# Performance work log

Hardware: AMD Instinct MI355X
Metric: run time of the kernel (lower is better)

## Reference

```python
import math
import jax, jax.numpy as jnp
import numpy as np

L, H, E, D = 12, 12, 768, 64   # stack_size, mh_size, embedding_dim, dim_w_matrices
B, S = 4, 512
EPS = 1e-5


def positional_enc(seq_len, model_dim):
    # faithful: power_ind = 10000 XOR int(2*i/dim)
    i = np.arange(model_dim)
    p = np.bitwise_xor(10000, (2 * i) // model_dim).astype(np.float32)
    pos = np.arange(seq_len, dtype=np.float32)[:, None]
    ang = pos / p[None, :]
    pe = np.where(i % 2 == 0, np.sin(ang), np.cos(ang)).astype(np.float32)
    return jnp.asarray(pe)


def layer_norm(x, g, b):
    mu = jnp.mean(x, axis=-1, keepdims=True)
    var = jnp.mean(jnp.square(x - mu), axis=-1, keepdims=True)
    return (x - mu) * jax.lax.rsqrt(var + EPS) * g + b


def encoder(x, wq, wo, g1, b1, fw, fb, g2, b2):
    # x: [B,S,E]; wq: [H,E,D]; wo: [E,H*D]; fw: [E,E] (torch Linear layout)
    bs = x.shape[0] * x.shape[1]
    nb = x.reshape(bs, E)                              # flatten batch (faithful)
    q = jnp.einsum('ne,hed->hnd', nb, wq)              # q == k == v (bug kept)
    scores = jax.nn.softmax(jnp.einsum('hnd,hmd->hnm', q, q) / math.sqrt(D), axis=-1)
    z = jnp.einsum('hnm,hmd->hnd', scores, q)          # [H,BS,D]
    zc = z.reshape(H * D, bs)                          # per-head view(D,-1) + cat
    mh = (wo @ zc).reshape(x.shape)                    # [B,S,E]
    l1 = layer_norm(x + mh, g1, b1)
    ffn = l1 @ fw.T + fb
    return layer_norm(l1 + ffn, g2, b2)


def setup_inputs() -> dict:
    key = jax.random.key(0)
    ks = jax.random.split(key, 8)

    def xavier(k, shape, fan_in, fan_out):
        lim = math.sqrt(6.0 / (fan_in + fan_out))
        return jax.random.uniform(k, shape, jnp.float32, -lim, lim)

    return {
        'tokens': jax.random.normal(ks[0], (B, S, E), jnp.float32),
        'wq':    xavier(ks[1], (L, H, E, D), E, D),
        'wo':    xavier(ks[2], (L, E, H * D), E, H * D),
        'ln1_g': jnp.ones((L, E), jnp.float32),
        'ln1_b': jnp.zeros((L, E), jnp.float32),
        'ffn_w': xavier(ks[3], (L, E, E), E, E),
        'ffn_b': jnp.zeros((L, E), jnp.float32),
        'ln2_g': jnp.ones((L, E), jnp.float32),
        'ln2_b': jnp.zeros((L, E), jnp.float32),
    }


def reference(tokens, wq, wo, ln1_g, ln1_b, ffn_w, ffn_b, ln2_g, ln2_b):
    pe = positional_enc(tokens.shape[1], tokens.shape[2])
    # faithful: layer 0 applied once on pe+tokens, then ALL layers (0 again) in loop
    x = encoder(pe + tokens, wq[0], wo[0], ln1_g[0], ln1_b[0],
                ffn_w[0], ffn_b[0], ln2_g[0], ln2_b[0])
    for l in range(L):
        x = encoder(x, wq[l], wo[l], ln1_g[l], ln1_b[l],
                    ffn_w[l], ffn_b[l], ln2_g[l], ln2_b[l])
    return x
```

## Files before the change

### kernel.cpp

```cpp
#include <hip/hip_runtime.h>
#include <hip/hip_bf16.h>


#define BS_TOK 2048
#define EMB 768
#define NH 12
#define HD 64
#define WQN (12 * NH * EMB * HD)

typedef __attribute__((ext_vector_type(8))) short bf16x8;
typedef __attribute__((ext_vector_type(4))) float f32x4;

__device__ __forceinline__ short f2bf(float f) {
  union { float f; unsigned u; } v;
  v.f = f;
  unsigned r = (v.u + 0x7FFF + ((v.u >> 16) & 1)) >> 16;
  return (short)(unsigned short)r;
}

#define MFMA16(a, b, c) __builtin_amdgcn_mfma_f32_16x16x32_bf16(a, b, c, 0, 0, 0)
#define SW64(r, k) ((r) * 64 + ((((k) >> 3) ^ ((r) & 7)) << 3) + ((k) & 7))

__global__ __launch_bounds__(256) void cvt_f32_bf16_kernel(const float* __restrict__ src,
                                                           short* __restrict__ dst) {
  int i = (blockIdx.x * 256 + threadIdx.x) * 8;
  float4 a = *(const float4*)(src + i);
  float4 b = *(const float4*)(src + i + 4);
  bf16x8 t;
  t[0] = f2bf(a.x); t[1] = f2bf(a.y); t[2] = f2bf(a.z); t[3] = f2bf(a.w);
  t[4] = f2bf(b.x); t[5] = f2bf(b.y); t[6] = f2bf(b.z); t[7] = f2bf(b.w);
  *(bf16x8*)(dst + i) = t;
}

__global__ __launch_bounds__(256) void wq_trans_kernel(const float* __restrict__ wq,
                                                       short* __restrict__ wqT) {
  __shared__ short T[64 * 64];
  const int et = blockIdx.x;
  const int lh = blockIdx.y;
  const int tid = threadIdx.x;
  const float* src = wq + ((size_t)lh * EMB + et * 64) * HD;
  {
    int r = tid >> 2, c16 = (tid & 3) << 4;
    const float* p = src + r * HD + c16;
    float4 x0 = *(const float4*)(p + 0);
    float4 x1 = *(const float4*)(p + 4);
    float4 x2 = *(const float4*)(p + 8);
    float4 x3 = *(const float4*)(p + 12);
    bf16x8 a, b;
    a[0] = f2bf(x0.x); a[1] = f2bf(x0.y); a[2] = f2bf(x0.z); a[3] = f2bf(x0.w);
    a[4] = f2bf(x1.x); a[5] = f2bf(x1.y); a[6] = f2bf(x1.z); a[7] = f2bf(x1.w);
    b[0] = f2bf(x2.x); b[1] = f2bf(x2.y); b[2] = f2bf(x2.z); b[3] = f2bf(x2.w);
    b[4] = f2bf(x3.x); b[5] = f2bf(x3.y); b[6] = f2bf(x3.z); b[7] = f2bf(x3.w);
    int g = c16 >> 3;
    *(bf16x8*)&T[r * 64 + ((g ^ (r & 7)) << 3)] = a;
    *(bf16x8*)&T[r * 64 + (((g + 1) ^ (r & 7)) << 3)] = b;
  }
  __syncthreads();
  {
    int d = tid >> 2, e16 = (tid & 3) << 4;
    bf16x8 t0, t1;
#pragma unroll
    for (int j = 0; j < 8; ++j) t0[j] = T[SW64(e16 + j, d)];
#pragma unroll
    for (int j = 0; j < 8; ++j) t1[j] = T[SW64(e16 + 8 + j, d)];
    short* q = wqT + ((size_t)lh * HD + d) * EMB + et * 64 + e16;
    *(bf16x8*)(q) = t0;
    *(bf16x8*)(q + 8) = t1;
  }
}

__global__ __launch_bounds__(256) void pe_add_kernel(const float* __restrict__ tok,
                                                     float* __restrict__ X,
                                                     short* __restrict__ Xb) {
  int idx = blockIdx.x * 256 + threadIdx.x;
  int e = idx % EMB;
  int t = idx / EMB;
  int s = t & 511;
  float p = (e < 384) ? 10000.0f : 10001.0f;
  float ang = (float)s / p;
  float pe = (e & 1) ? cosf(ang) : sinf(ang);
  float v = tok[idx] + pe;
  X[idx] = v;
  Xb[idx] = f2bf(v);
}

__device__ __forceinline__ void stage_direct_bf16(const short* __restrict__ src, int ld,
                                                  int row0, int k0, short* dst, int tid) {
  int r = tid >> 2, kb = (tid & 3) << 4;
  const short* p = src + (size_t)(row0 + r) * ld + k0 + kb;
  bf16x8 x0 = *(const bf16x8*)(p);
  bf16x8 x1 = *(const bf16x8*)(p + 8);
  int g = kb >> 3;
  *(bf16x8*)&dst[r * 64 + ((g ^ (r & 7)) << 3)] = x0;
  *(bf16x8*)&dst[r * 64 + (((g + 1) ^ (r & 7)) << 3)] = x1;
}

__device__ __forceinline__ void stage_trans_bf16(const short* __restrict__ src, int ld,
                                                 int k0, int col0, short* dst, int tid) {
  int kk = tid >> 2, nb = (tid & 3) << 4;
  const short* p = src + (size_t)(k0 + kk) * ld + col0 + nb;
  bf16x8 x0 = *(const bf16x8*)(p + 0);
  bf16x8 x1 = *(const bf16x8*)(p + 8);
#pragma unroll
  for (int j = 0; j < 8; ++j) dst[SW64(nb + j, kk)] = x0[j];
#pragma unroll
  for (int j = 0; j < 8; ++j) dst[SW64(nb + 8 + j, kk)] = x1[j];
}

#define GEMM_TILE_COMPUTE(As, Bs, acc)                                              \
  {                                                                                 \
    _Pragma("unroll") for (int s = 0; s < 2; ++s) {                                 \
      int ra = (w << 4) + l15;                                                      \
      bf16x8 af = *(const bf16x8*)&As[ra * 64 + ((((s << 2) + quad) ^ (ra & 7)) << 3)]; \
      _Pragma("unroll") for (int nt = 0; nt < 4; ++nt) {                            \
        int rb = (nt << 4) + l15;                                                   \
        bf16x8 bf = *(const bf16x8*)&Bs[rb * 64 + ((((s << 2) + quad) ^ (rb & 7)) << 3)]; \
        acc[nt] = MFMA16(af, bf, acc[nt]);                                          \
      }                                                                             \
    }                                                                               \
  }

__global__ __launch_bounds__(256) void gemm_q_kernel(const short* __restrict__ Xb,
                                                     const short* __restrict__ WqT,
                                                     short* __restrict__ Qo,
                                                     short* __restrict__ Qt) {
  __shared__ short As[64 * 64];
  __shared__ short Bs[64 * 64];
  const int m0 = blockIdx.x * 64;
  const int h = blockIdx.y;
  const int tid = threadIdx.x;
  const int w = tid >> 6, lane = tid & 63, l15 = lane & 15, quad = lane >> 4;
  const short* wqh = WqT + (size_t)h * (HD * EMB);
  f32x4 acc[4] = {(f32x4){0, 0, 0, 0}, (f32x4){0, 0, 0, 0},
                  (f32x4){0, 0, 0, 0}, (f32x4){0, 0, 0, 0}};
  for (int k0 = 0; k0 < EMB; k0 += 64) {
    stage_direct_bf16(Xb, EMB, m0, k0, As, tid);
    stage_direct_bf16(wqh, EMB, 0, k0, Bs, tid);
    __syncthreads();
    GEMM_TILE_COMPUTE(As, Bs, acc);
    __syncthreads();
  }
  short* qo = Qo + (size_t)h * (BS_TOK * HD);
#pragma unroll
  for (int nt = 0; nt < 4; ++nt)
#pragma unroll
    for (int r = 0; r < 4; ++r) {
      short v = f2bf(acc[nt][r]);
      int tokr = (w << 4) + (quad << 2) + r;
      int d = (nt << 4) + l15;
      qo[(size_t)(m0 + tokr) * HD + d] = v;
      As[SW64(tokr, d)] = v;
    }
  __syncthreads();
  {
    int d = tid >> 2, tok0 = (tid & 3) << 4;
    bf16x8 t0, t1;
#pragma unroll
    for (int j = 0; j < 8; ++j) t0[j] = As[SW64(tok0 + j, d)];
#pragma unroll
    for (int j = 0; j < 8; ++j) t1[j] = As[SW64(tok0 + 8 + j, d)];
    short* qt = Qt + (size_t)h * (HD * BS_TOK) + (size_t)d * BS_TOK + m0 + tok0;
    *(bf16x8*)(qt) = t0;
    *(bf16x8*)(qt + 8) = t1;
  }
}

__global__ __launch_bounds__(128) void attn_mfma_kernel(const short* __restrict__ Q,
                                                        const short* __restrict__ Qt,
                                                        float* __restrict__ Opart,
                                                        float* __restrict__ Lpart) {
  __shared__ short Ks[64 * 64];
  __shared__ short Vt[64 * 64];
  __shared__ short Pw[2 * 16 * 64];
  const int h = blockIdx.y;
  const int q0 = blockIdx.x * 32;
  const int kt0 = blockIdx.z * 16;
  const int tid = threadIdx.x;
  const int lane = tid & 63;
  const int wv = tid >> 6;
  const int l15 = lane & 15;
  const int quad = lane >> 4;
  const short* Qh = Q + (size_t)h * (BS_TOK * HD);
  const short* Qth = Qt + (size_t)h * (HD * BS_TOK);
  short* myP = Pw + wv * 16 * 64;

  bf16x8 qf[2];
  {
    const short* qp = Qh + (size_t)(q0 + wv * 16 + l15) * HD + quad * 8;
    qf[0] = *(const bf16x8*)(qp);
    qf[1] = *(const bf16x8*)(qp + 32);
  }

  f32x4 o[4];
  float lp[4] = {0.f, 0.f, 0.f, 0.f};
#pragma unroll
  for (int r = 0; r < 4; ++r) o[r] = (f32x4){0.f, 0.f, 0.f, 0.f};

  bf16x8 kreg[4], vreg[4];
#pragma unroll
  for (int i = 0; i < 4; ++i) {
    int c = i * 128 + tid;
    kreg[i] = *(const bf16x8*)(Qh + kt0 * 4096 + c * 8);
    vreg[i] = *(const bf16x8*)(Qth + (c >> 3) * BS_TOK + kt0 * 64 + (c & 7) * 8);
  }

  for (int kt = 0; kt < 16; ++kt) {
    __syncthreads();
#pragma unroll
    for (int i = 0; i < 4; ++i) {
      int c = i * 128 + tid, row = c >> 3, g = c & 7;
      *(bf16x8*)&Ks[row * 64 + ((g ^ (row & 7)) << 3)] = kreg[i];
      *(bf16x8*)&Vt[row * 64 + ((g ^ (row & 7)) << 3)] = vreg[i];
    }
    __syncthreads();
    if (kt < 15) {
      int gt = kt0 + kt + 1;
#pragma unroll
      for (int i = 0; i < 4; ++i) {
        int c = i * 128 + tid;
        kreg[i] = *(const bf16x8*)(Qh + gt * 4096 + c * 8);
        vreg[i] = *(const bf16x8*)(Qth + (c >> 3) * BS_TOK + gt * 64 + (c & 7) * 8);
      }
    }

    f32x4 s[4];
#pragma unroll
    for (int ct = 0; ct < 4; ++ct) {
      f32x4 acc = (f32x4){0.f, 0.f, 0.f, 0.f};
#pragma unroll
      for (int ks = 0; ks < 2; ++ks) {
        int row = ct * 16 + l15;
        int c = ks * 4 + quad;
        bf16x8 kf = *(const bf16x8*)(&Ks[row * 64 + ((c ^ (row & 7)) << 3)]);
        acc = MFMA16(qf[ks], kf, acc);
      }
      s[ct] = acc;
    }

#pragma unroll
    for (int ct = 0; ct < 4; ++ct)
#pragma unroll
      for (int r = 0; r < 4; ++r) {
        float p = __expf(s[ct][r] * 0.125f);
        lp[r] += p;
        myP[SW64(quad * 4 + r, ct * 16 + l15)] = f2bf(p);
      }

#pragma unroll
    for (int ks = 0; ks < 2; ++ks) {
      int c = ks * 4 + quad;
      bf16x8 pf = *(const bf16x8*)(&myP[l15 * 64 + ((c ^ (l15 & 7)) << 3)]);
#pragma unroll
      for (int dt = 0; dt < 4; ++dt) {
        int row = dt * 16 + l15;
        bf16x8 vf = *(const bf16x8*)(&Vt[row * 64 + ((c ^ (row & 7)) << 3)]);
        o[dt] = MFMA16(pf, vf, o[dt]);
      }
    }
  }

#pragma unroll
  for (int r = 0; r < 4; ++r) {
    float t = lp[r];
#pragma unroll
    for (int d = 1; d < 16; d <<= 1) t += __shfl_xor(t, d, 64);
    lp[r] = t;
  }
  float* Oh = Opart + ((size_t)blockIdx.z * NH + h) * (size_t)(BS_TOK * HD);
  float* Lh = Lpart + ((size_t)blockIdx.z * NH + h) * BS_TOK;
#pragma unroll
  for (int r = 0; r < 4; ++r) {
    int qrow = q0 + wv * 16 + quad * 4 + r;
#pragma unroll
    for (int dt = 0; dt < 4; ++dt)
      Oh[(size_t)qrow * HD + dt * 16 + l15] = o[dt][r];
    if (l15 == 0) Lh[qrow] = lp[r];
  }
}

__global__ __launch_bounds__(256) void attn_combine_kernel(const float* __restrict__ Op,
                                                           const float* __restrict__ Lp,
                                                           short* __restrict__ Z) {
  const int NBH = NH * BS_TOK * HD;
  int idx = blockIdx.x * 256 + threadIdx.x;
  float o = Op[idx] + Op[idx + NBH];
  int hq = idx >> 6;
  float l = Lp[hq] + Lp[hq + NH * BS_TOK];
  Z[idx] = f2bf(o / l);
}

__global__ __launch_bounds__(256) void gemm_out_kernel(const short* __restrict__ Wob,
                                                       const short* __restrict__ Zc,
                                                       float* __restrict__ MH) {
  __shared__ short As[64 * 64];
  __shared__ short Bs[64 * 64];
  const int n0 = blockIdx.x * 64;
  const int m0 = blockIdx.y * 64;
  const int tid = threadIdx.x;
  const int w = tid >> 6, lane = tid & 63, l15 = lane & 15, quad = lane >> 4;
  f32x4 acc[4] = {(f32x4){0, 0, 0, 0}, (f32x4){0, 0, 0, 0},
                  (f32x4){0, 0, 0, 0}, (f32x4){0, 0, 0, 0}};
  for (int k0 = 0; k0 < EMB; k0 += 64) {
    stage_direct_bf16(Wob, EMB, m0, k0, As, tid);
    stage_trans_bf16(Zc, BS_TOK, k0, n0, Bs, tid);
    __syncthreads();
    GEMM_TILE_COMPUTE(As, Bs, acc);
    __syncthreads();
  }
#pragma unroll
  for (int nt = 0; nt < 4; ++nt)
#pragma unroll
    for (int r = 0; r < 4; ++r)
      MH[(size_t)(m0 + (w << 4) + (quad << 2) + r) * BS_TOK + n0 + (nt << 4) + l15] =
          acc[nt][r];
}

__global__ __launch_bounds__(256) void gemm_ffn_kernel(const short* __restrict__ L1b,
                                                       const short* __restrict__ Fwb,
                                                       const float* __restrict__ Fb,
                                                       float* __restrict__ Out) {
  __shared__ short As[64 * 64];
  __shared__ short Bs[64 * 64];
  const int m0 = blockIdx.x * 64;
  const int n0 = blockIdx.y * 64;
  const int tid = threadIdx.x;
  const int w = tid >> 6, lane = tid & 63, l15 = lane & 15, quad = lane >> 4;
  f32x4 acc[4] = {(f32x4){0, 0, 0, 0}, (f32x4){0, 0, 0, 0},
                  (f32x4){0, 0, 0, 0}, (f32x4){0, 0, 0, 0}};
  for (int k0 = 0; k0 < EMB; k0 += 64) {
    stage_direct_bf16(L1b, EMB, m0, k0, As, tid);
    stage_direct_bf16(Fwb, EMB, n0, k0, Bs, tid);
    __syncthreads();
    GEMM_TILE_COMPUTE(As, Bs, acc);
    __syncthreads();
  }
#pragma unroll
  for (int nt = 0; nt < 4; ++nt) {
    float bias = Fb[n0 + (nt << 4) + l15];
#pragma unroll
    for (int r = 0; r < 4; ++r)
      Out[(size_t)(m0 + (w << 4) + (quad << 2) + r) * EMB + n0 + (nt << 4) + l15] =
          acc[nt][r] + bias;
  }
}

__global__ __launch_bounds__(256) void ln_kernel(const float* __restrict__ Xa,
                                                 const float* __restrict__ Xb,
                                                 const float* __restrict__ g,
                                                 const float* __restrict__ bb,
                                                 float* __restrict__ Out,
                                                 short* __restrict__ Outb) {
  __shared__ float red[4];
  const int t = blockIdx.x;
  const int tid = threadIdx.x;
  float v[3];
  float s = 0.f;
#pragma unroll
  for (int i = 0; i < 3; ++i) {
    int e = tid + i * 256;
    v[i] = Xa[t * EMB + e] + Xb[t * EMB + e];
    s += v[i];
  }
#pragma unroll
  for (int o = 32; o > 0; o >>= 1) s += __shfl_xor(s, o, 64);
  if ((tid & 63) == 0) red[tid >> 6] = s;
  __syncthreads();
  float mu = (red[0] + red[1] + red[2] + red[3]) * (1.0f / EMB);
  float q = 0.f;
#pragma unroll
  for (int i = 0; i < 3; ++i) {
    float d = v[i] - mu;
    q += d * d;
  }
#pragma unroll
  for (int o = 32; o > 0; o >>= 1) q += __shfl_xor(q, o, 64);
  __syncthreads();
  if ((tid & 63) == 0) red[tid >> 6] = q;
  __syncthreads();
  float var = (red[0] + red[1] + red[2] + red[3]) * (1.0f / EMB);
  float r = rsqrtf(var + 1e-5f);
#pragma unroll
  for (int i = 0; i < 3; ++i) {
    int e = tid + i * 256;
    float res = (v[i] - mu) * r * g[e] + bb[e];
    Out[t * EMB + e] = res;
    Outb[t * EMB + e] = f2bf(res);
  }
}

extern "C" void kernel_launch(void* const* d_in, const int* in_sizes, int n_in,
                              void* d_out, int out_size, void* d_ws, size_t ws_size,
                              hipStream_t stream) {
  const float* tok = (const float*)d_in[0];
  const float* wq = (const float*)d_in[1];
  const float* wo = (const float*)d_in[2];
  const float* g1 = (const float*)d_in[3];
  const float* b1 = (const float*)d_in[4];
  const float* fw = (const float*)d_in[5];
  const float* fb = (const float*)d_in[6];
  const float* g2 = (const float*)d_in[7];
  const float* b2 = (const float*)d_in[8];
  const int NB = BS_TOK * EMB;
  float* bufA = (float*)d_ws;
  float* bufB = bufA + NB;
  float* bufC = bufB + NB;
  float* Opart = bufB;
  short* XbA = (short*)(bufC + NB);
  short* L1b = XbA + NB;
  short* Qbf = L1b + NB;
  short* Qtb = Qbf + NB;
  short* Zbf = Qtb + NB;
  short* wqTb = Zbf + NB;
  short* wob = wqTb + WQN;
  short* fwb = wob + WQN;
  float* Lpart = (float*)(fwb + WQN);

  cvt_f32_bf16_kernel<<<WQN / (256 * 8), 256, 0, stream>>>(wo, wob);
  cvt_f32_bf16_kernel<<<WQN / (256 * 8), 256, 0, stream>>>(fw, fwb);
  wq_trans_kernel<<<dim3(12, 12 * NH), 256, 0, stream>>>(wq, wqTb);
  pe_add_kernel<<<NB / 256, 256, 0, stream>>>(tok, bufA, XbA);
  for (int it = 0; it < 13; ++it) {
    int l = (it == 0) ? 0 : it - 1;
    gemm_q_kernel<<<dim3(32, NH), 256, 0, stream>>>(
        XbA, wqTb + (size_t)l * (NH * HD * EMB), Qbf, Qtb);
    attn_mfma_kernel<<<dim3(64, NH, 2), 128, 0, stream>>>(Qbf, Qtb, Opart, Lpart);
    attn_combine_kernel<<<NH * BS_TOK * HD / 256, 256, 0, stream>>>(Opart, Lpart, Zbf);
    gemm_out_kernel<<<dim3(32, 12), 256, 0, stream>>>(
        wob + (size_t)l * (EMB * EMB), Zbf, bufB);
    ln_kernel<<<BS_TOK, 256, 0, stream>>>(bufA, bufB, g1 + l * EMB, b1 + l * EMB,
                                          bufC, L1b);
    gemm_ffn_kernel<<<dim3(32, 12), 256, 0, stream>>>(
        L1b, fwb + (size_t)l * (EMB * EMB), fb + l * EMB, bufB);
    float* ln2_dst = (it == 12) ? (float*)d_out : bufA;
    ln_kernel<<<BS_TOK, 256, 0, stream>>>(bufC, bufB, g2 + l * EMB, b2 + l * EMB,
                                          ln2_dst, XbA);
  }
}
```

Measured before the change: 1.257 ms.

## Split-K the output and FFN GEMMs, widen attention key split to four

Attention now splits the key range four ways instead of two, and the combine kernel sums four partial results. The output and FFN GEMMs use 128-row tiles and a two-way split-K, writing two partial buffers that the layernorm kernel sums along with the residual. The two weight conversion kernels are merged into one launch. The goal is more blocks in flight on a GPU with many CUs, at the cost of more partial-result traffic and reduction work.

```diff
diff --git a/kernel.cpp b/kernel.cpp
--- a/kernel.cpp
+++ b/kernel.cpp
@@ -21,8 +21,12 @@
 #define MFMA16(a, b, c) __builtin_amdgcn_mfma_f32_16x16x32_bf16(a, b, c, 0, 0, 0)
 #define SW64(r, k) ((r) * 64 + ((((k) >> 3) ^ ((r) & 7)) << 3) + ((k) & 7))
 
-__global__ __launch_bounds__(256) void cvt_f32_bf16_kernel(const float* __restrict__ src,
-                                                           short* __restrict__ dst) {
+__global__ __launch_bounds__(256) void cvt_weights_kernel(const float* __restrict__ wo,
+                                                          const float* __restrict__ fw,
+                                                          short* __restrict__ wob,
+                                                          short* __restrict__ fwb) {
+  const float* src = blockIdx.y ? fw : wo;
+  short* dst = blockIdx.y ? fwb : wob;
   int i = (blockIdx.x * 256 + threadIdx.x) * 8;
   float4 a = *(const float4*)(src + i);
   float4 b = *(const float4*)(src + i + 4);
@@ -95,6 +99,21 @@
   *(bf16x8*)&dst[r * 64 + (((g + 1) ^ (r & 7)) << 3)] = x1;
 }
 
+__device__ __forceinline__ void stage_direct128(const short* __restrict__ src, int ld,
+                                                int row0, int k0, short* dst, int tid) {
+  int r = tid >> 1, kb = (tid & 1) << 5;
+  const short* p = src + (size_t)(row0 + r) * ld + k0 + kb;
+  bf16x8 x0 = *(const bf16x8*)(p);
+  bf16x8 x1 = *(const bf16x8*)(p + 8);
+  bf16x8 x2 = *(const bf16x8*)(p + 16);
+  bf16x8 x3 = *(const bf16x8*)(p + 24);
+  int g = kb >> 3;
+  *(bf16x8*)&dst[r * 64 + (((g + 0) ^ (r & 7)) << 3)] = x0;
+  *(bf16x8*)&dst[r * 64 + (((g + 1) ^ (r & 7)) << 3)] = x1;
+  *(bf16x8*)&dst[r * 64 + (((g + 2) ^ (r & 7)) << 3)] = x2;
+  *(bf16x8*)&dst[r * 64 + (((g + 3) ^ (r & 7)) << 3)] = x3;
+}
+
 __device__ __forceinline__ void stage_trans_bf16(const short* __restrict__ src, int ld,
                                                  int k0, int col0, short* dst, int tid) {
   int kk = tid >> 2, nb = (tid & 3) << 4;
@@ -120,6 +139,23 @@
     }                                                                               \
   }
 
+#define GEMM_TILE_COMPUTE2(As, Bs, acc)                                             \
+  {                                                                                 \
+    _Pragma("unroll") for (int s = 0; s < 2; ++s) {                                 \
+      bf16x8 af[2];                                                                 \
+      _Pragma("unroll") for (int u = 0; u < 2; ++u) {                               \
+        int ra = (w << 5) + (u << 4) + l15;                                         \
+        af[u] = *(const bf16x8*)&As[ra * 64 + ((((s << 2) + quad) ^ (ra & 7)) << 3)]; \
+      }                                                                             \
+      _Pragma("unroll") for (int nt = 0; nt < 4; ++nt) {                            \
+        int rb = (nt << 4) + l15;                                                   \
+        bf16x8 bf = *(const bf16x8*)&Bs[rb * 64 + ((((s << 2) + quad) ^ (rb & 7)) << 3)]; \
+        acc[0][nt] = MFMA16(af[0], bf, acc[0][nt]);                                 \
+        acc[1][nt] = MFMA16(af[1], bf, acc[1][nt]);                                 \
+      }                                                                             \
+    }                                                                               \
+  }
+
 __global__ __launch_bounds__(256) void gemm_q_kernel(const short* __restrict__ Xb,
                                                      const short* __restrict__ WqT,
                                                      short* __restrict__ Qo,
@@ -174,7 +210,7 @@
   __shared__ short Pw[2 * 16 * 64];
   const int h = blockIdx.y;
   const int q0 = blockIdx.x * 32;
-  const int kt0 = blockIdx.z * 16;
+  const int kt0 = blockIdx.z * 8;
   const int tid = threadIdx.x;
   const int lane = tid & 63;
   const int wv = tid >> 6;
@@ -204,7 +240,7 @@
     vreg[i] = *(const bf16x8*)(Qth + (c >> 3) * BS_TOK + kt0 * 64 + (c & 7) * 8);
   }
 
-  for (int kt = 0; kt < 16; ++kt) {
+  for (int kt = 0; kt < 8; ++kt) {
     __syncthreads();
 #pragma unroll
     for (int i = 0; i < 4; ++i) {
@@ -213,7 +249,7 @@
       *(bf16x8*)&Vt[row * 64 + ((g ^ (row & 7)) << 3)] = vreg[i];
     }
     __syncthreads();
-    if (kt < 15) {
+    if (kt < 7) {
       int gt = kt0 + kt + 1;
 #pragma unroll
       for (int i = 0; i < 4; ++i) {
@@ -266,7 +302,8 @@
     for (int d = 1; d < 16; d <<= 1) t += __shfl_xor(t, d, 64);
     lp[r] = t;
   }
-  float* Oh = Opart + ((size_t)blockIdx.z * NH + h) * (size_t)(BS_TOK * HD);
+  const int NB = BS_TOK * EMB;
+  float* Oh = Opart + (size_t)blockIdx.z * NB + (size_t)h * (BS_TOK * HD);
   float* Lh = Lpart + ((size_t)blockIdx.z * NH + h) * BS_TOK;
 #pragma unroll
   for (int r = 0; r < 4; ++r) {
@@ -281,76 +318,85 @@
 __global__ __launch_bounds__(256) void attn_combine_kernel(const float* __restrict__ Op,
                                                            const float* __restrict__ Lp,
                                                            short* __restrict__ Z) {
-  const int NBH = NH * BS_TOK * HD;
+  const int NB = BS_TOK * EMB;
+  const int NHT = NH * BS_TOK;
   int idx = blockIdx.x * 256 + threadIdx.x;
-  float o = Op[idx] + Op[idx + NBH];
+  float o = Op[idx] + Op[idx + NB] + Op[idx + 2 * NB] + Op[idx + 3 * NB];
   int hq = idx >> 6;
-  float l = Lp[hq] + Lp[hq + NH * BS_TOK];
+  float l = Lp[hq] + Lp[hq + NHT] + Lp[hq + 2 * NHT] + Lp[hq + 3 * NHT];
   Z[idx] = f2bf(o / l);
 }
 
 __global__ __launch_bounds__(256) void gemm_out_kernel(const short* __restrict__ Wob,
                                                        const short* __restrict__ Zc,
-                                                       float* __restrict__ MH) {
-  __shared__ short As[64 * 64];
+                                                       float* __restrict__ Pp) {
+  __shared__ short As[128 * 64];
   __shared__ short Bs[64 * 64];
   const int n0 = blockIdx.x * 64;
-  const int m0 = blockIdx.y * 64;
+  const int m0 = blockIdx.y * 128;
+  const int kz = blockIdx.z * 384;
   const int tid = threadIdx.x;
   const int w = tid >> 6, lane = tid & 63, l15 = lane & 15, quad = lane >> 4;
-  f32x4 acc[4] = {(f32x4){0, 0, 0, 0}, (f32x4){0, 0, 0, 0},
-                  (f32x4){0, 0, 0, 0}, (f32x4){0, 0, 0, 0}};
-  for (int k0 = 0; k0 < EMB; k0 += 64) {
-    stage_direct_bf16(Wob, EMB, m0, k0, As, tid);
-    stage_trans_bf16(Zc, BS_TOK, k0, n0, Bs, tid);
-    __syncthreads();
-    GEMM_TILE_COMPUTE(As, Bs, acc);
-    __syncthreads();
-  }
-#pragma unroll
-  for (int nt = 0; nt < 4; ++nt)
-#pragma unroll
-    for (int r = 0; r < 4; ++r)
-      MH[(size_t)(m0 + (w << 4) + (quad << 2) + r) * BS_TOK + n0 + (nt << 4) + l15] =
-          acc[nt][r];
+  f32x4 acc[2][4] = {};
+  for (int k0 = 0; k0 < 384; k0 += 64) {
+    stage_direct128(Wob, EMB, m0, kz + k0, As, tid);
+    stage_trans_bf16(Zc, BS_TOK, kz + k0, n0, Bs, tid);
+    __syncthreads();
+    GEMM_TILE_COMPUTE2(As, Bs, acc);
+    __syncthreads();
+  }
+  float* P = Pp + (size_t)blockIdx.z * (BS_TOK * EMB);
+#pragma unroll
+  for (int u = 0; u < 2; ++u)
+#pragma unroll
+    for (int nt = 0; nt < 4; ++nt)
+#pragma unroll
+      for (int r = 0; r < 4; ++r)
+        P[(size_t)(m0 + (w << 5) + (u << 4) + (quad << 2) + r) * BS_TOK + n0 +
+          (nt << 4) + l15] = acc[u][nt][r];
 }
 
 __global__ __launch_bounds__(256) void gemm_ffn_kernel(const short* __restrict__ L1b,
                                                        const short* __restrict__ Fwb,
                                                        const float* __restrict__ Fb,
-                                                       float* __restrict__ Out) {
-  __shared__ short As[64 * 64];
+                                                       float* __restrict__ Pp) {
+  __shared__ short As[128 * 64];
   __shared__ short Bs[64 * 64];
-  const int m0 = blockIdx.x * 64;
+  const int m0 = blockIdx.x * 128;
   const int n0 = blockIdx.y * 64;
+  const int kz = blockIdx.z * 384;
   const int tid = threadIdx.x;
   const int w = tid >> 6, lane = tid & 63, l15 = lane & 15, quad = lane >> 4;
-  f32x4 acc[4] = {(f32x4){0, 0, 0, 0}, (f32x4){0, 0, 0, 0},
-                  (f32x4){0, 0, 0, 0}, (f32x4){0, 0, 0, 0}};
-  for (int k0 = 0; k0 < EMB; k0 += 64) {
-    stage_direct_bf16(L1b, EMB, m0, k0, As, tid);
-    stage_direct_bf16(Fwb, EMB, n0, k0, Bs, tid);
-    __syncthreads();
-    GEMM_TILE_COMPUTE(As, Bs, acc);
-    __syncthreads();
-  }
+  f32x4 acc[2][4] = {};
+  for (int k0 = 0; k0 < 384; k0 += 64) {
+    stage_direct128(L1b, EMB, m0, kz + k0, As, tid);
+    stage_direct_bf16(Fwb, EMB, n0, kz + k0, Bs, tid);
+    __syncthreads();
+    GEMM_TILE_COMPUTE2(As, Bs, acc);
+    __syncthreads();
+  }
+  float* P = Pp + (size_t)blockIdx.z * (BS_TOK * EMB);
+  const bool addb = (blockIdx.z == 0);
 #pragma unroll
   for (int nt = 0; nt < 4; ++nt) {
-    float bias = Fb[n0 + (nt << 4) + l15];
-#pragma unroll
-    for (int r = 0; r < 4; ++r)
-      Out[(size_t)(m0 + (w << 4) + (quad << 2) + r) * EMB + n0 + (nt << 4) + l15] =
-          acc[nt][r] + bias;
+    float bias = addb ? Fb[n0 + (nt << 4) + l15] : 0.0f;
+#pragma unroll
+    for (int u = 0; u < 2; ++u)
+#pragma unroll
+      for (int r = 0; r < 4; ++r)
+        P[(size_t)(m0 + (w << 5) + (u << 4) + (quad << 2) + r) * EMB + n0 +
+          (nt << 4) + l15] = acc[u][nt][r] + bias;
   }
 }
 
 __global__ __launch_bounds__(256) void ln_kernel(const float* __restrict__ Xa,
-                                                 const float* __restrict__ Xb,
+                                                 const float* __restrict__ P,
                                                  const float* __restrict__ g,
                                                  const float* __restrict__ bb,
                                                  float* __restrict__ Out,
                                                  short* __restrict__ Outb) {
   __shared__ float red[4];
+  const int NB = BS_TOK * EMB;
   const int t = blockIdx.x;
   const int tid = threadIdx.x;
   float v[3];
@@ -358,7 +404,8 @@
 #pragma unroll
   for (int i = 0; i < 3; ++i) {
     int e = tid + i * 256;
-    v[i] = Xa[t * EMB + e] + Xb[t * EMB + e];
+    int idx = t * EMB + e;
+    v[i] = Xa[idx] + P[idx] + P[idx + NB];
     s += v[i];
   }
 #pragma unroll
@@ -404,8 +451,9 @@
   float* bufA = (float*)d_ws;
   float* bufB = bufA + NB;
   float* bufC = bufB + NB;
-  float* Opart = bufB;
-  short* XbA = (short*)(bufC + NB);
+  float* bufD = bufC + NB;
+  float* bufE = bufD + NB;
+  short* XbA = (short*)(bufE + NB);
   short* L1b = XbA + NB;
   short* Qbf = L1b + NB;
   short* Qtb = Qbf + NB;
@@ -415,24 +463,23 @@
   short* fwb = wob + WQN;
   float* Lpart = (float*)(fwb + WQN);
 
-  cvt_f32_bf16_kernel<<<WQN / (256 * 8), 256, 0, stream>>>(wo, wob);
-  cvt_f32_bf16_kernel<<<WQN / (256 * 8), 256, 0, stream>>>(fw, fwb);
+  cvt_weights_kernel<<<dim3(WQN / (256 * 8), 2), 256, 0, stream>>>(wo, fw, wob, fwb);
   wq_trans_kernel<<<dim3(12, 12 * NH), 256, 0, stream>>>(wq, wqTb);
   pe_add_kernel<<<NB / 256, 256, 0, stream>>>(tok, bufA, XbA);
   for (int it = 0; it < 13; ++it) {
     int l = (it == 0) ? 0 : it - 1;
     gemm_q_kernel<<<dim3(32, NH), 256, 0, stream>>>(
         XbA, wqTb + (size_t)l * (NH * HD * EMB), Qbf, Qtb);
-    attn_mfma_kernel<<<dim3(64, NH, 2), 128, 0, stream>>>(Qbf, Qtb, Opart, Lpart);
-    attn_combine_kernel<<<NH * BS_TOK * HD / 256, 256, 0, stream>>>(Opart, Lpart, Zbf);
-    gemm_out_kernel<<<dim3(32, 12), 256, 0, stream>>>(
+    attn_mfma_kernel<<<dim3(64, NH, 4), 128, 0, stream>>>(Qbf, Qtb, bufB, Lpart);
+    attn_combine_kernel<<<NB / 256, 256, 0, stream>>>(bufB, Lpart, Zbf);
+    gemm_out_kernel<<<dim3(32, 6, 2), 256, 0, stream>>>(
         wob + (size_t)l * (EMB * EMB), Zbf, bufB);
     ln_kernel<<<BS_TOK, 256, 0, stream>>>(bufA, bufB, g1 + l * EMB, b1 + l * EMB,
-                                          bufC, L1b);
-    gemm_ffn_kernel<<<dim3(32, 12), 256, 0, stream>>>(
+                                          bufD, L1b);
+    gemm_ffn_kernel<<<dim3(16, 12, 2), 256, 0, stream>>>(
         L1b, fwb + (size_t)l * (EMB * EMB), fb + l * EMB, bufB);
     float* ln2_dst = (it == 12) ? (float*)d_out : bufA;
-    ln_kernel<<<BS_TOK, 256, 0, stream>>>(bufC, bufB, g2 + l * EMB, b2 + l * EMB,
+    ln_kernel<<<BS_TOK, 256, 0, stream>>>(bufD, bufB, g2 + l * EMB, b2 + l * EMB,
                                           ln2_dst, XbA);
   }
 }
```

Measured after the change: 1.305 ms. 1.04x slower.
